# Kernel optimization log

Measured on AMD Instinct MI355X. Metric: run time of the kernel, lower is better.

The kernel has to match this reference:

```python
import jax, jax.numpy as jnp
import numpy as np

H = 512
V_SRC = 32000
V_TGT = 32000
B = 64
S = 128


def setup_inputs() -> dict:
    key = jax.random.key(0)
    ks = jax.random.split(key, 16)
    sc = 0.02
    embed_src = (jax.random.normal(ks[0], (V_SRC, H), jnp.float32) * sc).at[0].set(0.0)
    embed_tgt = (jax.random.normal(ks[1], (V_TGT, H), jnp.float32) * sc).at[0].set(0.0)
    return {
        "source": jax.random.randint(ks[2], (B, S), 0, V_SRC),
        "target": jax.random.randint(ks[3], (B, S), 0, V_TGT),
        "embed_src": embed_src,
        "embed_tgt": embed_tgt,
        "enc_Wih": jax.random.normal(ks[4], (4 * H, H), jnp.float32) * sc,
        "enc_Whh": jax.random.normal(ks[5], (4 * H, H), jnp.float32) * sc,
        "enc_bih": jnp.zeros((4 * H,), jnp.float32),
        "enc_bhh": jnp.zeros((4 * H,), jnp.float32),
        "dec_Wih": jax.random.normal(ks[6], (4 * H, H), jnp.float32) * sc,
        "dec_Whh": jax.random.normal(ks[7], (4 * H, H), jnp.float32) * sc,
        "dec_bih": jnp.zeros((4 * H,), jnp.float32),
        "dec_bhh": jnp.zeros((4 * H,), jnp.float32),
        "attn_W": jax.random.normal(ks[8], (H, 2 * H), jnp.float32) * sc,
        "attn_b": jnp.zeros((H,), jnp.float32),
        "out_W": jax.random.normal(ks[9], (V_TGT, H), jnp.float32) * sc,
        "out_b": jnp.zeros((V_TGT,), jnp.float32),
    }


def _lstm_step(x, h, c, Wih, Whh, bih, bhh):
    gates = x @ Wih.T + h @ Whh.T + bih + bhh  # [B, 4H]
    i, f, g, o = jnp.split(gates, 4, axis=-1)
    c2 = jax.nn.sigmoid(f) * c + jax.nn.sigmoid(i) * jnp.tanh(g)
    h2 = jax.nn.sigmoid(o) * jnp.tanh(c2)
    return h2, c2


def reference(source, target, embed_src, embed_tgt,
              enc_Wih, enc_Whh, enc_bih, enc_bhh,
              dec_Wih, dec_Whh, dec_bih, dec_bhh,
              attn_W, attn_b, out_W, out_b):
    b, s = source.shape
    src_t = source.T  # [S, B]
    tgt_t = target.T  # [S, B]

    h0 = jnp.zeros((b, H), jnp.float32)

    def enc_step(carry, words):
        h, c = carry
        x = embed_src[words]                       # [B, H]
        h2, c2 = _lstm_step(x, h, c, enc_Wih, enc_Whh, enc_bih, enc_bhh)
        m = (words != 0)[:, None]                  # keep old state at PAD
        h2 = jnp.where(m, h2, h)
        c2 = jnp.where(m, c2, c)
        return (h2, c2), h2

    (eh, ec), enc_hs = jax.lax.scan(enc_step, (h0, h0), src_t)  # enc_hs: [S, B, H]
    src_mask = (src_t != 0)[:, :, None]            # [S, B, 1]

    steps_f = tgt_t[: s - 1]  # decoder length tied to source length per original code
    steps_t = tgt_t[1:]

    def dec_step(carry, wt):
        h, c, loss = carry
        words_f, word_t = wt
        x = embed_tgt[words_f]
        h2, c2 = _lstm_step(x, h, c, dec_Wih, dec_Whh, dec_bih, dec_bhh)
        m = (words_f != 0)[:, None]
        h2 = jnp.where(m, h2, h)
        c2 = jnp.where(m, c2, c)
        # dot-product attention over encoder states, softmax over source dim
        scores = jnp.sum(h2[None] * enc_hs, axis=-1, keepdims=True)  # [S, B, 1]
        scores = jnp.where(src_mask, scores, -jnp.inf)
        aw = jax.nn.softmax(scores, axis=0)
        ctx = jnp.sum(aw * enc_hs, axis=0)                           # [B, H]
        ha = jnp.tanh(jnp.concatenate([ctx, h2], axis=1) @ attn_W.T + attn_b)
        logits = ha @ out_W.T + out_b                                # [B, V]
        logp = jax.nn.log_softmax(logits, axis=-1)
        tok = -jnp.take_along_axis(logp, word_t[:, None], axis=1)[:, 0]
        valid = (word_t != 0)
        step_loss = jnp.sum(jnp.where(valid, tok, 0.0)) / jnp.maximum(valid.sum(), 1).astype(jnp.float32)
        return (h2, c2, loss + step_loss), None

    (_, _, loss), _ = jax.lax.scan(dec_step, (eh, ec, jnp.float32(0.0)), (steps_f, steps_t))
    return loss[None]  # shape (1,), matching unsqueeze(0)
```

## Files before the change

kernel.cpp:

```cpp
#include <hip/hip_runtime.h>
#include <hip/hip_bf16.h>
#include <math.h>

typedef __attribute__((ext_vector_type(8))) short bf16x8;
typedef __attribute__((ext_vector_type(8))) unsigned short ushort8;
typedef __attribute__((ext_vector_type(4))) float f32x4;

#define NLSTM 32
#define ATTN0 32
#define NATTN 64
#define HA0   96
#define NHA   8
#define LOG0  104
#define NLOG  125
#define NBLK  229

#define FL_LSTM 0
#define FL_ATTN 32
#define FL_CTX  64
#define FL_HA   128
#define FL_LOGD 136

static __device__ inline unsigned short f2bf(float f) {
    unsigned u = __builtin_bit_cast(unsigned, f);
    u += 0x7fffu + ((u >> 16) & 1u);
    return (unsigned short)(u >> 16);
}
static __device__ inline float bf2f(unsigned short u) {
    return __builtin_bit_cast(float, ((unsigned)u) << 16);
}

__device__ inline ushort8 llc_load8_wait(const unsigned short* p) {
    ushort8 v;
    asm volatile("global_load_dwordx4 %0, %1, off sc0 sc1\n\ts_waitcnt vmcnt(0)"
                 : "=v"(v) : "v"(p) : "memory");
    return v;
}
#define LLC_LOAD8_ISSUE(dst, p) \
    asm volatile("global_load_dwordx4 %0, %1, off sc0 sc1" : "=v"(dst) : "v"(p))
#define VMCNT0() do { asm volatile("s_waitcnt vmcnt(0)" ::: "memory"); \
                      __builtin_amdgcn_sched_barrier(0); } while (0)
__device__ inline void llc_store16(unsigned short* p, unsigned short v) {
    unsigned uv = v;
    asm volatile("global_store_short %0, %1, off sc0 sc1" :: "v"(p), "v"(uv) : "memory");
}
__device__ inline void llc_store32(void* p, unsigned v) {
    asm volatile("global_store_dword %0, %1, off sc0 sc1" :: "v"(p), "v"(v) : "memory");
}
__device__ inline void llc_storef(float* p, float v) {
    asm volatile("global_store_dword %0, %1, off sc0 sc1" :: "v"(p), "v"(__builtin_bit_cast(unsigned, v)) : "memory");
}

__device__ inline void poll_flags(const unsigned* fl, int mask, unsigned target) {
    if (threadIdx.x < 64) {
        const unsigned* p = fl + (threadIdx.x & mask) * 32;
        while (true) {
            unsigned v;
            asm volatile("global_load_dword %0, %1, off sc0 sc1\n\ts_waitcnt vmcnt(0)"
                         : "=v"(v) : "v"(p) : "memory");
            if (__all((int)(v >= target))) break;
            __builtin_amdgcn_s_sleep(1);
        }
    }
    __syncthreads();
}

__device__ inline void drain_sync() {
    asm volatile("s_waitcnt vmcnt(0)" ::: "memory");
    __syncthreads();
}

__device__ inline void wait_count(unsigned* f, unsigned target) {
    if (threadIdx.x == 0) {
        while (__hip_atomic_load(f, __ATOMIC_RELAXED, __HIP_MEMORY_SCOPE_AGENT) < target)
            __builtin_amdgcn_s_sleep(4);
    }
    __syncthreads();
}

__device__ inline void signal_count(unsigned* f) {
    drain_sync();
    if (threadIdx.x == 0)
        __hip_atomic_fetch_add(f, 1u, __ATOMIC_RELAXED, __HIP_MEMORY_SCOPE_AGENT);
}


__global__ void conv_lstm_w2(unsigned short* dstX, unsigned short* dstH,
                             const float* __restrict__ Wih,
                             const float* __restrict__ Whh) {
    int idx = blockIdx.x * 256 + threadIdx.x;
    int np = idx >> 9, k = idx & 511;
    int h = np >> 2, g = np & 3;
    int src = (g * 512 + h) * 512 + k;
    dstX[idx] = f2bf(Wih[src]);
    dstH[idx] = f2bf(Whh[src]);
}

__global__ void conv_plain(unsigned short* dst, const float* __restrict__ src, int n) {
    int idx = blockIdx.x * 256 + threadIdx.x;
    if (idx < n) dst[idx] = f2bf(src[idx]);
}

__global__ __launch_bounds__(256) void xw_kernel(
    const int* __restrict__ source, const int* __restrict__ target,
    const float* __restrict__ embS, const float* __restrict__ embT,
    const float* __restrict__ ebih, const float* __restrict__ ebhh,
    const float* __restrict__ dbih, const float* __restrict__ dbhh,
    const unsigned short* __restrict__ WxE, const unsigned short* __restrict__ WxD,
    unsigned short* __restrict__ xwb)
{
    __shared__ unsigned short xh[64 * 264];
    __shared__ int words_sm[64];
    const int s = blockIdx.x >> 5, sub = blockIdx.x & 31;
    const bool enc = (s < 128);
    const int col = enc ? s : (s - 128);
    const int* wsrc = enc ? source : target;
    const float* embed = enc ? embS : embT;
    const unsigned short* Wx = enc ? WxE : WxD;
    const float* b1 = enc ? ebih : dbih;
    const float* b2 = enc ? ebhh : dbhh;
    const int tid = threadIdx.x, lane = tid & 63, wave = tid >> 6;
    const int wm = wave >> 1, wn = wave & 1, l16 = lane & 15, lq = lane >> 4;
    const int n0 = sub * 64;
    if (tid < 64) words_sm[tid] = wsrc[tid * 128 + col];
    f32x4 acc[2][2] = {};
    for (int kt = 0; kt < 2; ++kt) {
        __syncthreads();
        for (int i = 0; i < 16; ++i) {
            int e4 = i * 256 + tid;
            int row = e4 >> 6, kloc = (e4 & 63) * 4;
            float4 v = *(const float4*)(embed + (long)words_sm[row] * 512 + kt * 256 + kloc);
            ushort4 sv;
            sv.x = f2bf(v.x); sv.y = f2bf(v.y); sv.z = f2bf(v.z); sv.w = f2bf(v.w);
            *(ushort4*)&xh[row * 264 + kloc] = sv;
        }
        __syncthreads();
        for (int ks = 0; ks < 8; ++ks) {
            bf16x8 a[2], b[2];
            for (int mt = 0; mt < 2; ++mt)
                a[mt] = *(const bf16x8*)&xh[(wm * 32 + mt * 16 + l16) * 264 + ks * 32 + lq * 8];
            for (int nt = 0; nt < 2; ++nt)
                b[nt] = *(const bf16x8*)(Wx + (long)(n0 + wn * 32 + nt * 16 + l16) * 512 + kt * 256 + ks * 32 + lq * 8);
            for (int mt = 0; mt < 2; ++mt)
                for (int nt = 0; nt < 2; ++nt)
                    acc[mt][nt] = __builtin_amdgcn_mfma_f32_16x16x32_bf16(a[mt], b[nt], acc[mt][nt], 0, 0, 0);
        }
    }
    for (int mt = 0; mt < 2; ++mt)
        for (int nt = 0; nt < 2; ++nt)
            for (int r = 0; r < 4; ++r) {
                int m = wm * 32 + mt * 16 + lq * 4 + r;
                int ng = n0 + wn * 32 + nt * 16 + l16;
                int bi = ((ng & 3) << 9) | (ng >> 2);
                float val = acc[mt][nt][r] + b1[bi] + b2[bi];
                xwb[((long)s * 64 + m) * 2048 + ng] = f2bf(val);
            }
}

__device__ void lstm_phase(int bid,
    const unsigned short* __restrict__ Wh,
    const unsigned short* __restrict__ xwt,
    const int* __restrict__ words,
    const unsigned short* __restrict__ hp,
    float* __restrict__ c_buf,
    unsigned short* __restrict__ h_out,
    char* smem_raw)
{
    unsigned short* xh    = (unsigned short*)smem_raw;
    float* gsm            = (float*)(smem_raw + 33792);
    int* words_sm         = (int*)(smem_raw + 50432);
    unsigned short* hp_sm = (unsigned short*)(smem_raw + 50688);
    unsigned short* xw_sm = (unsigned short*)(smem_raw + 52736);
    const int tid = threadIdx.x, lane = tid & 63, wave = tid >> 6;
    const int wm = wave >> 1, wn = wave & 1, l16 = lane & 15, lq = lane >> 4;
    const int n0 = bid * 64, h0 = bid * 16;

    if (tid < 64) words_sm[tid] = words[tid * 128];

    ushort8 tA[8], tB[8], xwr[2];
    if (hp) {
        #pragma unroll
        for (int i = 0; i < 8; ++i) {
            int e8 = i * 256 + tid;
            LLC_LOAD8_ISSUE(tA[i], hp + (e8 >> 5) * 512 + (e8 & 31) * 8);
        }
        #pragma unroll
        for (int i = 0; i < 8; ++i) {
            int e8 = i * 256 + tid;
            LLC_LOAD8_ISSUE(tB[i], hp + (e8 >> 5) * 512 + 256 + (e8 & 31) * 8);
        }
    } else {
        #pragma unroll
        for (int i = 0; i < 8; ++i) { tA[i] = (ushort8)0; tB[i] = (ushort8)0; }
    }
    #pragma unroll
    for (int i = 0; i < 2; ++i) {
        int e8 = i * 256 + tid;
        LLC_LOAD8_ISSUE(xwr[i], xwt + (e8 >> 3) * 2048 + n0 + (e8 & 7) * 8);
    }
    VMCNT0();
    #pragma unroll
    for (int i = 0; i < 2; ++i) {
        int e8 = i * 256 + tid;
        *(ushort8*)&xw_sm[(e8 >> 3) * 68 + (e8 & 7) * 8] = xwr[i];
    }
    #pragma unroll
    for (int i = 0; i < 8; ++i) {
        int e8 = i * 256 + tid;
        *(ushort8*)&xh[(e8 >> 5) * 264 + (e8 & 31) * 8] = tA[i];
    }
    __syncthreads();

    f32x4 acc[2][2] = {};
    #pragma unroll
    for (int ks = 0; ks < 8; ++ks) {
        bf16x8 a[2], b[2];
        for (int mt = 0; mt < 2; ++mt)
            a[mt] = *(const bf16x8*)&xh[(wm * 32 + mt * 16 + l16) * 264 + ks * 32 + lq * 8];
        for (int nt = 0; nt < 2; ++nt)
            b[nt] = *(const bf16x8*)(Wh + (long)(n0 + wn * 32 + nt * 16 + l16) * 512 + ks * 32 + lq * 8);
        for (int mt = 0; mt < 2; ++mt)
            for (int nt = 0; nt < 2; ++nt)
                acc[mt][nt] = __builtin_amdgcn_mfma_f32_16x16x32_bf16(a[mt], b[nt], acc[mt][nt], 0, 0, 0);
    }
    if (h0 < 256 && tid < 128)
        *(ushort8*)&hp_sm[(tid >> 1) * 16 + (tid & 1) * 8] =
            *(const ushort8*)&xh[(tid >> 1) * 264 + h0 + (tid & 1) * 8];
    __syncthreads();
    #pragma unroll
    for (int i = 0; i < 8; ++i) {
        int e8 = i * 256 + tid;
        *(ushort8*)&xh[(e8 >> 5) * 264 + (e8 & 31) * 8] = tB[i];
    }
    __syncthreads();
    #pragma unroll
    for (int ks = 0; ks < 8; ++ks) {
        bf16x8 a[2], b[2];
        for (int mt = 0; mt < 2; ++mt)
            a[mt] = *(const bf16x8*)&xh[(wm * 32 + mt * 16 + l16) * 264 + ks * 32 + lq * 8];
        for (int nt = 0; nt < 2; ++nt)
            b[nt] = *(const bf16x8*)(Wh + (long)(n0 + wn * 32 + nt * 16 + l16) * 512 + 256 + ks * 32 + lq * 8);
        for (int mt = 0; mt < 2; ++mt)
            for (int nt = 0; nt < 2; ++nt)
                acc[mt][nt] = __builtin_amdgcn_mfma_f32_16x16x32_bf16(a[mt], b[nt], acc[mt][nt], 0, 0, 0);
    }
    if (h0 >= 256 && tid < 128)
        *(ushort8*)&hp_sm[(tid >> 1) * 16 + (tid & 1) * 8] =
            *(const ushort8*)&xh[(tid >> 1) * 264 + (h0 - 256) + (tid & 1) * 8];
    for (int mt = 0; mt < 2; ++mt)
        for (int nt = 0; nt < 2; ++nt)
            for (int r = 0; r < 4; ++r) {
                int m = wm * 32 + mt * 16 + lq * 4 + r;
                int n = wn * 32 + nt * 16 + l16;
                gsm[m * 65 + n] = acc[mt][nt][r];
            }
    __syncthreads();

    for (int q = 0; q < 2; ++q) {
        int it = q * 256 + tid;
        int b = it >> 3, hl = (it & 7) * 2;
        int hg = h0 + hl;
        ushort4 xg0 = *(const ushort4*)&xw_sm[b * 68 + hl * 4];
        ushort4 xg1 = *(const ushort4*)&xw_sm[b * 68 + hl * 4 + 4];
        float i0 = gsm[b * 65 + hl * 4 + 0] + bf2f(xg0.x);
        float f0 = gsm[b * 65 + hl * 4 + 1] + bf2f(xg0.y);
        float g0 = gsm[b * 65 + hl * 4 + 2] + bf2f(xg0.z);
        float o0 = gsm[b * 65 + hl * 4 + 3] + bf2f(xg0.w);
        float i1 = gsm[b * 65 + hl * 4 + 4] + bf2f(xg1.x);
        float f1 = gsm[b * 65 + hl * 4 + 5] + bf2f(xg1.y);
        float g1 = gsm[b * 65 + hl * 4 + 6] + bf2f(xg1.z);
        float o1 = gsm[b * 65 + hl * 4 + 7] + bf2f(xg1.w);
        float c0old = c_buf[b * 512 + hg], c1old = c_buf[b * 512 + hg + 1];
        float c0 = (1.f / (1.f + __expf(-f0))) * c0old + (1.f / (1.f + __expf(-i0))) * tanhf(g0);
        float c1 = (1.f / (1.f + __expf(-f1))) * c1old + (1.f / (1.f + __expf(-i1))) * tanhf(g1);
        float h0v = (1.f / (1.f + __expf(-o0))) * tanhf(c0);
        float h1v = (1.f / (1.f + __expf(-o1))) * tanhf(c1);
        bool masked = (words_sm[b] == 0);
        unsigned short hb0 = masked ? hp_sm[b * 16 + hl]     : f2bf(h0v);
        unsigned short hb1 = masked ? hp_sm[b * 16 + hl + 1] : f2bf(h1v);
        float2 cw;
        cw.x = masked ? c0old : c0;
        cw.y = masked ? c1old : c1;
        *(float2*)&c_buf[b * 512 + hg] = cw;
        llc_store32(h_out + b * 512 + hg, (unsigned)hb0 | ((unsigned)hb1 << 16));
    }
}

__device__ void attn_phase(int b,
    const unsigned short* __restrict__ dh,
    const unsigned short* __restrict__ enc_hs,
    const int* __restrict__ source,
    unsigned short* __restrict__ ctx,
    char* smem_raw)
{
    float* h2s = (float*)smem_raw;
    float* sc  = (float*)(smem_raw + 2048);
    const int tid = threadIdx.x;
    if (tid < 64) {
        ushort8 v = llc_load8_wait(dh + b * 512 + tid * 8);
        #pragma unroll
        for (int j = 0; j < 8; ++j) h2s[tid * 8 + j] = bf2f(v[j]);
    }
    __syncthreads();
    const int wave = tid >> 6, lane = tid & 63;
    for (int i = 0; i < 32; ++i) {
        int tt = wave * 32 + i;
        ushort8 ev = *(const ushort8*)(enc_hs + ((long)tt * 64 + b) * 512 + lane * 8);
        const float* hq = h2s + lane * 8;
        float v = 0.f;
        #pragma unroll
        for (int j = 0; j < 8; ++j) v += bf2f(ev[j]) * hq[j];
        for (int off = 32; off; off >>= 1) v += __shfl_xor(v, off);
        if (lane == 0) sc[tt] = (source[b * 128 + tt] != 0) ? v : -1e30f;
    }
    __syncthreads();
    if (tid < 64) {
        float s0 = sc[tid], s1 = sc[tid + 64];
        float mx = fmaxf(s0, s1);
        for (int off = 32; off; off >>= 1) mx = fmaxf(mx, __shfl_xor(mx, off));
        float e0 = __expf(s0 - mx), e1 = __expf(s1 - mx);
        float sm = e0 + e1;
        for (int off = 32; off; off >>= 1) sm += __shfl_xor(sm, off);
        sc[tid] = e0 / sm;
        sc[tid + 64] = e1 / sm;
    }
    __syncthreads();
    float a0 = 0.f, a1 = 0.f;
    #pragma unroll 4
    for (int tt = 0; tt < 128; ++tt) {
        float w = sc[tt];
        unsigned pv = *(const unsigned*)(enc_hs + ((long)tt * 64 + b) * 512 + tid * 2);
        a0 += w * bf2f((unsigned short)(pv & 0xffff));
        a1 += w * bf2f((unsigned short)(pv >> 16));
    }
    unsigned pk = (unsigned)f2bf(a0) | ((unsigned)f2bf(a1) << 16);
    llc_store32(ctx + b * 512 + tid * 2, pk);
}

#define HA_WRITE(reg) do { _Pragma("unroll") \
    for (int i = 0; i < 8; ++i) { int e8 = i * 256 + tid; \
        *(ushort8*)&xh[(e8 >> 5) * 264 + (e8 & 31) * 8] = reg[i]; } } while (0)
#define HA_ISSUE(reg, srcp, koff) do { _Pragma("unroll") \
    for (int i = 0; i < 8; ++i) { int e8 = i * 256 + tid; \
        LLC_LOAD8_ISSUE(reg[i], (srcp) + (e8 >> 5) * 512 + (koff) + (e8 & 31) * 8); } } while (0)
#define HA_MFMA(kt) do { _Pragma("unroll") \
    for (int ks = 0; ks < 8; ++ks) { \
        bf16x8 a[2], b[2]; \
        for (int mt = 0; mt < 2; ++mt) \
            a[mt] = *(const bf16x8*)&xh[(wm * 32 + mt * 16 + l16) * 264 + ks * 32 + lq * 8]; \
        for (int nt = 0; nt < 2; ++nt) \
            b[nt] = *(const bf16x8*)(Wa + (long)(n0 + wn * 32 + nt * 16 + l16) * 1024 + (kt) * 256 + ks * 32 + lq * 8); \
        for (int mt = 0; mt < 2; ++mt) \
            for (int nt = 0; nt < 2; ++nt) \
                acc[mt][nt] = __builtin_amdgcn_mfma_f32_16x16x32_bf16(a[mt], b[nt], acc[mt][nt], 0, 0, 0); \
    } } while (0)

__device__ void ha_phase(int bid,
    const unsigned short* __restrict__ ctx,
    const unsigned short* __restrict__ dh,
    const unsigned short* __restrict__ Wa,
    const float* __restrict__ ab,
    unsigned short* __restrict__ ha,
    char* smem_raw)
{
    unsigned short* xh = (unsigned short*)smem_raw;
    const int tid = threadIdx.x, lane = tid & 63, wave = tid >> 6;
    const int wm = wave >> 1, wn = wave & 1, l16 = lane & 15, lq = lane >> 4;
    const int n0 = bid * 64;
    f32x4 acc[2][2] = {};
    ushort8 rA[8], rB[8];
    HA_ISSUE(rA, ctx, 0);
    HA_ISSUE(rB, ctx, 256);
    VMCNT0();
    HA_WRITE(rA); __syncthreads();
    HA_ISSUE(rA, dh, 0);
    HA_MFMA(0); __syncthreads();
    HA_WRITE(rB); __syncthreads();
    HA_ISSUE(rB, dh, 256);
    HA_MFMA(1); __syncthreads();
    VMCNT0();
    HA_WRITE(rA); __syncthreads();
    HA_MFMA(2); __syncthreads();
    HA_WRITE(rB); __syncthreads();
    HA_MFMA(3);
    for (int mt = 0; mt < 2; ++mt)
        for (int nt = 0; nt < 2; ++nt)
            for (int r = 0; r < 4; ++r) {
                int m = wm * 32 + mt * 16 + lq * 4 + r;
                int n = n0 + wn * 32 + nt * 16 + l16;
                llc_store16(ha + m * 512 + n, f2bf(tanhf(acc[mt][nt][r] + ab[n])));
            }
}

__device__ void logits_phase(int bid, int tt,
    const unsigned short* __restrict__ ha,
    const unsigned short* __restrict__ Wo,
    const float* __restrict__ ob,
    const int* __restrict__ target,
    float* __restrict__ sumexp,
    float* __restrict__ logit_t,
    char* smem_raw)
{
    float* se = (float*)smem_raw;
    const int tid = threadIdx.x, lane = tid & 63, wave = tid >> 6;
    const int wm = wave >> 1, wn = wave & 1;
    const int l16 = lane & 15, lq = lane >> 4;
    const int n0 = bid * 256;
    f32x4 acc[2][8] = {};
    for (int ks = 0; ks < 16; ++ks) {
        bf16x8 a[2];
        for (int mt = 0; mt < 2; ++mt)
            a[mt] = *(const bf16x8*)(ha + (wm * 32 + mt * 16 + l16) * 512 + ks * 32 + lq * 8);
        for (int nt = 0; nt < 8; ++nt) {
            int v = n0 + wn * 128 + nt * 16 + l16;
            bf16x8 bb = *(const bf16x8*)(Wo + (long)v * 512 + ks * 32 + lq * 8);
            for (int mt = 0; mt < 2; ++mt)
                acc[mt][nt] = __builtin_amdgcn_mfma_f32_16x16x32_bf16(a[mt], bb, acc[mt][nt], 0, 0, 0);
        }
    }
    if (tid < 64) se[tid] = 0.f;
    __syncthreads();
    for (int mt = 0; mt < 2; ++mt) {
        for (int r = 0; r < 4; ++r) {
            int b = wm * 32 + mt * 16 + lq * 4 + r;
            int tw = target[b * 128 + tt + 1];
            float partial = 0.f;
            for (int nt = 0; nt < 8; ++nt) {
                int n = n0 + wn * 128 + nt * 16 + l16;
                float val = acc[mt][nt][r] + ob[n];
                partial += __expf(val);
                if (n == tw) llc_storef(logit_t + tt * 64 + b, val);
            }
            for (int m = 1; m < 16; m <<= 1) partial += __shfl_xor(partial, m);
            if (l16 == 0) atomicAdd(&se[b], partial);
        }
    }
    __syncthreads();
    if (tid < 64) atomicAdd(&sumexp[tt * 64 + tid], se[tid]);
}

__device__ void loss_phase(const float* __restrict__ sumexp,
                           const float* __restrict__ logit_t,
                           const int* __restrict__ target,
                           float* __restrict__ out,
                           char* smem_raw)
{
    float* red = (float*)smem_raw;
    const int tid = threadIdx.x;
    float local = 0.f;
    if (tid < 127) {
        float s = 0.f; int cnt = 0;
        for (int b = 0; b < 64; ++b) {
            int w = target[b * 128 + tid + 1];
            if (w != 0) {
                s += logf(sumexp[tid * 64 + b]) - logit_t[tid * 64 + b];
                cnt++;
            }
        }
        int c = cnt > 1 ? cnt : 1;
        local = s / (float)c;
    }
    if (tid < 128) red[tid] = local;
    __syncthreads();
    if (tid == 0) {
        float tot = 0.f;
        for (int i = 0; i < 127; ++i) tot += red[i];
        out[0] = tot;
    }
}

__global__ __launch_bounds__(256) void seq_kernel(
    const int* __restrict__ source, const int* __restrict__ target,
    const float* __restrict__ attnb, const float* __restrict__ outb,
    const unsigned short* __restrict__ WhE, const unsigned short* __restrict__ WhD,
    const unsigned short* __restrict__ Wattn, const unsigned short* __restrict__ Wout,
    const unsigned short* __restrict__ xwb,
    unsigned short* enc_hs, unsigned short* dec_h, unsigned short* ctx,
    unsigned short* ha_t, float* c_buf, float* sumexp, float* logit_t,
    float* out, unsigned* flags)
{
    __shared__ __align__(16) char smem[61440];
    const int bid = blockIdx.x;
    const int tid = threadIdx.x;

    unsigned* flLstm = flags + FL_LSTM * 32;
    unsigned* flAttn = flags + FL_ATTN * 32;
    unsigned* flCtx  = flags + FL_CTX  * 32;
    unsigned* flHa   = flags + FL_HA   * 32;
    unsigned* logDone = flags + FL_LOGD * 32;

    if (bid < NLSTM) {
        int h0 = bid * 16;
        for (int q = 0; q < 4; ++q) {
            int it = q * 256 + tid;
            c_buf[(it & 63) * 512 + h0 + (it >> 6)] = 0.f;
        }
        for (int t = 0; t < 128; ++t) {
            if (t) poll_flags(flLstm, 31, (unsigned)t);
            lstm_phase(bid, WhE, xwb + (long)t * 131072, source + t,
                       t ? enc_hs + (long)(t - 1) * 32768 : nullptr,
                       c_buf, enc_hs + (long)t * 32768, smem);
            drain_sync();
            if (tid == 0) {
                llc_store32(&flLstm[bid * 32], (unsigned)(t + 1));
                llc_store32(&flAttn[bid * 32], (unsigned)(t + 1));
            }
        }
        for (int t = 0; t < 127; ++t) {
            poll_flags(flLstm, 31, (unsigned)(128 + t));
            lstm_phase(bid, WhD, xwb + (long)(128 + t) * 131072, target + t,
                       t ? dec_h + (long)(t - 1) * 32768 : enc_hs + (long)127 * 32768,
                       c_buf, dec_h + (long)t * 32768, smem);
            drain_sync();
            if (tid == 0) {
                llc_store32(&flLstm[bid * 32], (unsigned)(129 + t));
                llc_store32(&flAttn[bid * 32], (unsigned)(129 + t));
            }
        }
        if (bid == 0) {
            wait_count(logDone, (unsigned)NLOG);
            loss_phase(sumexp, logit_t, target, out, smem);
        }
    } else if (bid < ATTN0 + NATTN) {
        const int col = bid - ATTN0;
        for (int t = 0; t < 127; ++t) {
            poll_flags(flAttn, 31, (unsigned)(129 + t));
            attn_phase(col, dec_h + (long)t * 32768, enc_hs, source,
                       ctx + (long)t * 32768, smem);
            drain_sync();
            if (tid == 0) llc_store32(&flCtx[col * 32], (unsigned)(t + 1));
        }
    } else if (bid < HA0 + NHA) {
        const int sub = bid - HA0;
        for (int t = 0; t < 127; ++t) {
            poll_flags(flCtx, 63, (unsigned)(t + 1));
            ha_phase(sub, ctx + (long)t * 32768, dec_h + (long)t * 32768,
                     Wattn, attnb, ha_t + (long)t * 32768, smem);
            drain_sync();
            if (tid == 0) llc_store32(&flHa[sub * 32], (unsigned)(t + 1));
        }
    } else {
        const int sub = bid - LOG0;
        for (int t = 0; t < 127; ++t) {
            poll_flags(flHa, 7, (unsigned)(t + 1));
            logits_phase(sub, t, ha_t + (long)t * 32768, Wout, outb,
                         target, sumexp, logit_t, smem);
        }
        signal_count(logDone);
    }
}

extern "C" void kernel_launch(void* const* d_in, const int* in_sizes, int n_in,
                              void* d_out, int out_size, void* d_ws, size_t ws_size,
                              hipStream_t stream)
{
    (void)in_sizes; (void)n_in; (void)out_size; (void)ws_size;
    const int*   source = (const int*)  d_in[0];
    const int*   target = (const int*)  d_in[1];
    const float* embS   = (const float*)d_in[2];
    const float* embT   = (const float*)d_in[3];
    const float* eWih   = (const float*)d_in[4];
    const float* eWhh   = (const float*)d_in[5];
    const float* ebih   = (const float*)d_in[6];
    const float* ebhh   = (const float*)d_in[7];
    const float* dWih   = (const float*)d_in[8];
    const float* dWhh   = (const float*)d_in[9];
    const float* dbih   = (const float*)d_in[10];
    const float* dbhh   = (const float*)d_in[11];
    const float* attnW  = (const float*)d_in[12];
    const float* attnb  = (const float*)d_in[13];
    const float* outW   = (const float*)d_in[14];
    const float* outb   = (const float*)d_in[15];
    float* out = (float*)d_out;
    char* ws = (char*)d_ws;

    unsigned short* enc_hs = (unsigned short*)(ws);
    unsigned short* ha_t   = (unsigned short*)(ws + 8388608);
    unsigned short* xwb    = (unsigned short*)(ws + 16777216);
    unsigned short* dec_h  = (unsigned short*)(ws + 16777216);
    unsigned short* ctx    = (unsigned short*)(ws + 25100288);
    float* c_buf           = (float*)(ws + 83623936);
    float* sumexp          = (float*)(ws + 83755008);
    float* logitt          = (float*)(ws + 83787776);
    unsigned short* WxE    = (unsigned short*)(ws + 83820544);
    unsigned short* WhE    = (unsigned short*)(ws + 85917696);
    unsigned short* WxD    = (unsigned short*)(ws + 88014848);
    unsigned short* WhD    = (unsigned short*)(ws + 90112000);
    unsigned short* Wattn  = (unsigned short*)(ws + 92209152);
    unsigned short* Wout   = (unsigned short*)(ws + 93257728);
    unsigned* flags        = (unsigned*)(ws + 126025728);

    hipMemsetAsync(flags, 0, 18432, stream);
    hipMemsetAsync(sumexp, 0, 32768, stream);
    conv_lstm_w2<<<4096, 256, 0, stream>>>(WxE, WhE, eWih, eWhh);
    conv_lstm_w2<<<4096, 256, 0, stream>>>(WxD, WhD, dWih, dWhh);
    conv_plain<<<2048, 256, 0, stream>>>(Wattn, attnW, 512 * 1024);
    conv_plain<<<64000, 256, 0, stream>>>(Wout, outW, 32000 * 512);
    xw_kernel<<<255 * 32, 256, 0, stream>>>(source, target, embS, embT,
                                            ebih, ebhh, dbih, dbhh, WxE, WxD, xwb);

    seq_kernel<<<NBLK, 256, 0, stream>>>(
        source, target, attnb, outb,
        WhE, WhD, Wattn, Wout, xwb,
        enc_hs, dec_h, ctx, ha_t, c_buf, sumexp, logitt,
        out, flags);
}
```

Baseline: 4.942 ms.

## Replace many-flag polling with aggregated generation flags and defer xw smem store

Consumer blocks (attention and logits) used to poll all 32 or 8 producer flags with a full wave. Now one aggregator (LSTM block 0, or HA block 0) polls the producers and publishes a generation counter to 8 replicated flag lines. Each consumer polls a single line with one thread, which cuts polling traffic to the LLC. The cost is an extra hop of latency on the critical path. Separately, the wait for the xw load in lstm_phase is relaxed to vmcnt(10), and its shared-memory store is moved later so it overlaps with the first MFMA half.

```diff
diff --git a/kernel.cpp b/kernel.cpp
--- a/kernel.cpp
+++ b/kernel.cpp
@@ -16,10 +16,11 @@
 #define NBLK  229
 
 #define FL_LSTM 0
-#define FL_ATTN 32
-#define FL_CTX  64
-#define FL_HA   128
-#define FL_LOGD 136
+#define FL_CTX  32
+#define FL_HA   96
+#define FL_DGR  104
+#define FL_LGR  112
+#define FL_LOGD 120
 
 static __device__ inline unsigned short f2bf(float f) {
     unsigned u = __builtin_bit_cast(unsigned, f);
@@ -40,6 +41,8 @@
     asm volatile("global_load_dwordx4 %0, %1, off sc0 sc1" : "=v"(dst) : "v"(p))
 #define VMCNT0() do { asm volatile("s_waitcnt vmcnt(0)" ::: "memory"); \
                       __builtin_amdgcn_sched_barrier(0); } while (0)
+#define WAITVM(N) do { asm volatile("s_waitcnt vmcnt(" #N ")" ::: "memory"); \
+                       __builtin_amdgcn_sched_barrier(0); } while (0)
 __device__ inline void llc_store16(unsigned short* p, unsigned short v) {
     unsigned uv = v;
     asm volatile("global_store_short %0, %1, off sc0 sc1" :: "v"(p), "v"(uv) : "memory");
@@ -59,6 +62,19 @@
             asm volatile("global_load_dword %0, %1, off sc0 sc1\n\ts_waitcnt vmcnt(0)"
                          : "=v"(v) : "v"(p) : "memory");
             if (__all((int)(v >= target))) break;
+            __builtin_amdgcn_s_sleep(1);
+        }
+    }
+    __syncthreads();
+}
+
+__device__ inline void poll_one(const unsigned* line, unsigned target) {
+    if (threadIdx.x == 0) {
+        while (true) {
+            unsigned v;
+            asm volatile("global_load_dword %0, %1, off sc0 sc1\n\ts_waitcnt vmcnt(0)"
+                         : "=v"(v) : "v"(line) : "memory");
+            if (v >= target) break;
             __builtin_amdgcn_s_sleep(1);
         }
     }
@@ -198,12 +214,7 @@
         int e8 = i * 256 + tid;
         LLC_LOAD8_ISSUE(xwr[i], xwt + (e8 >> 3) * 2048 + n0 + (e8 & 7) * 8);
     }
-    VMCNT0();
-    #pragma unroll
-    for (int i = 0; i < 2; ++i) {
-        int e8 = i * 256 + tid;
-        *(ushort8*)&xw_sm[(e8 >> 3) * 68 + (e8 & 7) * 8] = xwr[i];
-    }
+    WAITVM(10);
     #pragma unroll
     for (int i = 0; i < 8; ++i) {
         int e8 = i * 256 + tid;
@@ -227,10 +238,16 @@
         *(ushort8*)&hp_sm[(tid >> 1) * 16 + (tid & 1) * 8] =
             *(const ushort8*)&xh[(tid >> 1) * 264 + h0 + (tid & 1) * 8];
     __syncthreads();
+    VMCNT0();
     #pragma unroll
     for (int i = 0; i < 8; ++i) {
         int e8 = i * 256 + tid;
         *(ushort8*)&xh[(e8 >> 5) * 264 + (e8 & 31) * 8] = tB[i];
+    }
+    #pragma unroll
+    for (int i = 0; i < 2; ++i) {
+        int e8 = i * 256 + tid;
+        *(ushort8*)&xw_sm[(e8 >> 3) * 68 + (e8 & 7) * 8] = xwr[i];
     }
     __syncthreads();
     #pragma unroll
@@ -484,9 +501,10 @@
     const int tid = threadIdx.x;
 
     unsigned* flLstm = flags + FL_LSTM * 32;
-    unsigned* flAttn = flags + FL_ATTN * 32;
     unsigned* flCtx  = flags + FL_CTX  * 32;
     unsigned* flHa   = flags + FL_HA   * 32;
+    unsigned* dgr    = flags + FL_DGR  * 32;
+    unsigned* lgr    = flags + FL_LGR  * 32;
     unsigned* logDone = flags + FL_LOGD * 32;
 
     if (bid < NLSTM) {
@@ -496,35 +514,36 @@
             c_buf[(it & 63) * 512 + h0 + (it >> 6)] = 0.f;
         }
         for (int t = 0; t < 128; ++t) {
-            if (t) poll_flags(flLstm, 31, (unsigned)t);
+            if (t) {
+                poll_flags(flLstm, 31, (unsigned)t);
+                if (bid == 0 && tid < 8) llc_store32(&dgr[tid * 32], (unsigned)t);
+            }
             lstm_phase(bid, WhE, xwb + (long)t * 131072, source + t,
                        t ? enc_hs + (long)(t - 1) * 32768 : nullptr,
                        c_buf, enc_hs + (long)t * 32768, smem);
             drain_sync();
-            if (tid == 0) {
-                llc_store32(&flLstm[bid * 32], (unsigned)(t + 1));
-                llc_store32(&flAttn[bid * 32], (unsigned)(t + 1));
-            }
+            if (tid == 0) llc_store32(&flLstm[bid * 32], (unsigned)(t + 1));
         }
         for (int t = 0; t < 127; ++t) {
             poll_flags(flLstm, 31, (unsigned)(128 + t));
+            if (bid == 0 && tid < 8) llc_store32(&dgr[tid * 32], (unsigned)(128 + t));
             lstm_phase(bid, WhD, xwb + (long)(128 + t) * 131072, target + t,
                        t ? dec_h + (long)(t - 1) * 32768 : enc_hs + (long)127 * 32768,
                        c_buf, dec_h + (long)t * 32768, smem);
             drain_sync();
-            if (tid == 0) {
-                llc_store32(&flLstm[bid * 32], (unsigned)(129 + t));
-                llc_store32(&flAttn[bid * 32], (unsigned)(129 + t));
-            }
+            if (tid == 0) llc_store32(&flLstm[bid * 32], (unsigned)(129 + t));
         }
         if (bid == 0) {
+            poll_flags(flLstm, 31, 255u);
+            if (tid < 8) llc_store32(&dgr[tid * 32], 255u);
             wait_count(logDone, (unsigned)NLOG);
             loss_phase(sumexp, logit_t, target, out, smem);
         }
     } else if (bid < ATTN0 + NATTN) {
         const int col = bid - ATTN0;
+        const unsigned* myGen = &dgr[(bid & 7) * 32];
         for (int t = 0; t < 127; ++t) {
-            poll_flags(flAttn, 31, (unsigned)(129 + t));
+            poll_one(myGen, (unsigned)(129 + t));
             attn_phase(col, dec_h + (long)t * 32768, enc_hs, source,
                        ctx + (long)t * 32768, smem);
             drain_sync();
@@ -538,11 +557,16 @@
                      Wattn, attnb, ha_t + (long)t * 32768, smem);
             drain_sync();
             if (tid == 0) llc_store32(&flHa[sub * 32], (unsigned)(t + 1));
+            if (sub == 0) {
+                poll_flags(flHa, 7, (unsigned)(t + 1));
+                if (tid < 8) llc_store32(&lgr[tid * 32], (unsigned)(t + 1));
+            }
         }
     } else {
         const int sub = bid - LOG0;
+        const unsigned* myGen = &lgr[(sub & 7) * 32];
         for (int t = 0; t < 127; ++t) {
-            poll_flags(flHa, 7, (unsigned)(t + 1));
+            poll_one(myGen, (unsigned)(t + 1));
             logits_phase(sub, t, ha_t + (long)t * 32768, Wout, outb,
                          target, sumexp, logit_t, smem);
         }
@@ -590,7 +614,7 @@
     unsigned short* Wout   = (unsigned short*)(ws + 93257728);
     unsigned* flags        = (unsigned*)(ws + 126025728);
 
-    hipMemsetAsync(flags, 0, 18432, stream);
+    hipMemsetAsync(flags, 0, 16384, stream);
     hipMemsetAsync(sumexp, 0, 32768, stream);
     conv_lstm_w2<<<4096, 256, 0, stream>>>(WxE, WhE, eWih, eWhh);
     conv_lstm_w2<<<4096, 256, 0, stream>>>(WxD, WhD, dWih, dWhh);
```

New measurement: 4.972 ms. No clear change (+0.6%).
